# Kernel optimization log

Hardware: AMD Instinct MI355X
Metric: run time of the kernel (lower is better)

Reference implementation:

```python
import jax, jax.numpy as jnp
import numpy as np

N = 50000      # nodes
E = 800000     # edges (before self-loops)
F_IN = 64      # num_features
HID = 32       # hidden_channels
HEADS = 4
CLS = 3
NEG_SLOPE = 0.2  # PyG GATConv default


def setup_inputs() -> dict:
    key = jax.random.key(0)
    ks = jax.random.split(key, 12)
    s = 0.1
    return {
        "x": jax.random.normal(ks[0], (N, F_IN), jnp.float32),
        "W1": jax.random.normal(ks[1], (F_IN, HEADS * HID), jnp.float32) * s,
        "att_src1": jax.random.normal(ks[2], (HEADS, HID), jnp.float32) * s,
        "att_dst1": jax.random.normal(ks[3], (HEADS, HID), jnp.float32) * s,
        "b1": jnp.zeros((HEADS * HID,), jnp.float32),
        "W2": jax.random.normal(ks[4], (HEADS * HID, HID), jnp.float32) * s,
        "att_src2": jax.random.normal(ks[5], (1, HID), jnp.float32) * s,
        "att_dst2": jax.random.normal(ks[6], (1, HID), jnp.float32) * s,
        "b2": jnp.zeros((HID,), jnp.float32),
        "linW": jax.random.normal(ks[7], (HID, CLS), jnp.float32) * s,
        "linb": jnp.zeros((CLS,), jnp.float32),
        "edge_index": jax.random.randint(ks[8], (2, E), 0, N, dtype=jnp.int64),
    }


def _gat_conv(x, W, att_src, att_dst, bias, src, dst, heads):
    """PyG GATConv (eval mode, self-loops pre-added in src/dst)."""
    n = x.shape[0]
    h = (x @ W).reshape(n, heads, -1)                      # [N,H,C]
    a_src = jnp.sum(h * att_src, axis=-1)                  # [N,H]
    a_dst = jnp.sum(h * att_dst, axis=-1)                  # [N,H]
    e = jax.nn.leaky_relu(a_src[src] + a_dst[dst], NEG_SLOPE)  # [E,H]
    # segment softmax over destination node
    m = jax.ops.segment_max(e, dst, num_segments=n)
    p = jnp.exp(e - m[dst])
    denom = jax.ops.segment_sum(p, dst, num_segments=n)
    alpha = p / denom[dst]                                 # [E,H]
    msg = h[src] * alpha[:, :, None]                       # [E,H,C]
    out = jax.ops.segment_sum(msg, dst, num_segments=n)    # [N,H,C]
    return out.reshape(n, -1) + bias                       # concat heads


def reference(x, W1, att_src1, att_dst1, b1, W2, att_src2, att_dst2, b2, linW, linb, edge_index):
    n = x.shape[0]
    loop = jnp.arange(n, dtype=edge_index.dtype)
    src = jnp.concatenate([edge_index[0], loop])  # add self-loops (PyG default)
    dst = jnp.concatenate([edge_index[1], loop])
    h = _gat_conv(x, W1, att_src1, att_dst1, b1, src, dst, HEADS)
    h = jax.nn.elu(h)
    h = _gat_conv(h, W2, att_src2, att_dst2, b2, src, dst, 1)
    g = jnp.mean(h, axis=0, keepdims=True)        # batch is None path
    logits = g @ linW + linb                      # [1, CLS]
    return jax.nn.softmax(logits, axis=1)
```

## Files before the change

### kernel.cpp

```cpp
#include <hip/hip_runtime.h>
#include <hip/hip_fp16.h>
#include <math.h>

#define NEG_SLOPE 0.2f
#define CAP 64
#define SCB 2048

static __device__ __forceinline__ void atomAdd(float* a, float v) {
    unsafeAtomicAdd(a, v);
}

static __device__ __forceinline__ bool edges_are_i64(const int* __restrict__ ei) {
    return (ei[1] | ei[3] | ei[5] | ei[7]) == 0;
}
static __device__ __forceinline__ int ldsrc(const int* __restrict__ ei, int e, int E, bool i64) {
    return i64 ? ei[2 * e] : ei[e];
}
static __device__ __forceinline__ int lddst(const int* __restrict__ ei, int e, int E, bool i64) {
    return i64 ? ei[2 * (E + e)] : ei[E + e];
}

__global__ __launch_bounds__(256) void scatter_k(const int* __restrict__ ei,
                                                 int* __restrict__ deg,
                                                 int* __restrict__ col, int E, int N) {
    const int tid = threadIdx.x;
    const int grp = blockIdx.x & 7;
    const int bin = blockIdx.x >> 3;
    const int nb  = gridDim.x >> 3;
    const bool i64 = edges_are_i64(ei);
    const int ET = E + N;
    const int d0 = (int)((long long)grp * N / 8);
    const int d1 = (int)((long long)(grp + 1) * N / 8);
    for (int e = bin * 256 + tid; e < ET; e += nb * 256) {
        int s, d;
        if (e < E) { s = ldsrc(ei, e, E, i64); d = lddst(ei, e, E, i64); }
        else       { s = d = e - E; }
        if (d >= d0 && d < d1) {
            int pos = atomicAdd(&deg[d], 1);
            if (pos < CAP) col[d * CAP + pos] = s;
        }
    }
}

__global__ __launch_bounds__(256, 4) void gemm1_k(const float* __restrict__ x,
                                                  const float* __restrict__ W,
                                                  const float* __restrict__ aws,
                                                  const float* __restrict__ awd,
                                                  __half* __restrict__ h,
                                                  float* __restrict__ as_,
                                                  float* __restrict__ ad_, int N) {
    __shared__ float Ws[64 * 128];
    __shared__ float xs[32 * 64];
    const int tid = threadIdx.x;
    const int cg = tid & 31, rg = tid >> 5;
    const int r0 = blockIdx.x * 32;
#pragma unroll 1
    for (int i = tid; i < 8192; i += 256) Ws[i] = W[i];
    {
        const float* src = x + (size_t)r0 * 64;
        const int limit = (N - r0) * 64;
#pragma unroll 1
        for (int i = tid * 4; i < 2048; i += 1024) {
            float4 v = (i < limit) ? *(const float4*)(src + i) : make_float4(0, 0, 0, 0);
            *(float4*)(xs + i) = v;
        }
    }
    __syncthreads();

    float acc[4][4] = {};
#pragma unroll 2
    for (int k = 0; k < 64; k += 4) {
        float4 w0 = *(const float4*)(Ws + (k + 0) * 128 + cg * 4);
        float4 w1 = *(const float4*)(Ws + (k + 1) * 128 + cg * 4);
        float4 w2 = *(const float4*)(Ws + (k + 2) * 128 + cg * 4);
        float4 w3 = *(const float4*)(Ws + (k + 3) * 128 + cg * 4);
        float4 xv[4];
#pragma unroll
        for (int q = 0; q < 4; ++q) xv[q] = *(const float4*)(xs + (rg * 4 + q) * 64 + k);
#pragma unroll
        for (int q = 0; q < 4; ++q) {
            float4 xq = xv[q];
            acc[q][0] += xq.x * w0.x + xq.y * w1.x + xq.z * w2.x + xq.w * w3.x;
            acc[q][1] += xq.x * w0.y + xq.y * w1.y + xq.z * w2.y + xq.w * w3.y;
            acc[q][2] += xq.x * w0.z + xq.y * w1.z + xq.z * w2.z + xq.w * w3.z;
            acc[q][3] += xq.x * w0.w + xq.y * w1.w + xq.z * w2.w + xq.w * w3.w;
        }
    }

    const int jbase = cg * 4;
    const int head = cg >> 3;
    const float a0 = aws[jbase], a1 = aws[jbase + 1], a2 = aws[jbase + 2], a3 = aws[jbase + 3];
    const float d0 = awd[jbase], d1 = awd[jbase + 1], d2 = awd[jbase + 2], d3 = awd[jbase + 3];
    float ps[4], pd[4];
#pragma unroll
    for (int q = 0; q < 4; ++q) {
        ps[q] = acc[q][0] * a0 + acc[q][1] * a1 + acc[q][2] * a2 + acc[q][3] * a3;
        pd[q] = acc[q][0] * d0 + acc[q][1] * d1 + acc[q][2] * d2 + acc[q][3] * d3;
        int row = r0 + rg * 4 + q;
        if (row < N) {
            __half hv[4];
            hv[0] = __float2half(acc[q][0]); hv[1] = __float2half(acc[q][1]);
            hv[2] = __float2half(acc[q][2]); hv[3] = __float2half(acc[q][3]);
            *(uint2*)(h + (size_t)row * 128 + jbase) = *(uint2*)hv;
        }
    }
#pragma unroll
    for (int off = 4; off; off >>= 1) {
#pragma unroll
        for (int q = 0; q < 4; ++q) {
            ps[q] += __shfl_down(ps[q], off, 8);
            pd[q] += __shfl_down(pd[q], off, 8);
        }
    }
    if ((cg & 7) == 0) {
#pragma unroll
        for (int q = 0; q < 4; ++q) {
            int row = r0 + rg * 4 + q;
            if (row < N) { as_[row * 4 + head] = ps[q]; ad_[row * 4 + head] = pd[q]; }
        }
    }
}

__global__ __launch_bounds__(256, 4) void gemm2_k(const float* __restrict__ hact,
                                                  const float* __restrict__ W,
                                                  const float* __restrict__ aws,
                                                  const float* __restrict__ awd,
                                                  __half* __restrict__ h2,
                                                  float* __restrict__ as_,
                                                  float* __restrict__ ad_, int N) {
    __shared__ float Ws[128 * 32];
    __shared__ float xs[128 * 68];
    const int tid = threadIdx.x;
    const int cg = tid & 7, rg = tid >> 3;
    const int r0 = blockIdx.x * 128;
    for (int i = tid; i < 4096; i += 256) Ws[i] = W[i];

    float acc[4][4] = {};
#pragma unroll 1
    for (int p = 0; p < 2; ++p) {
        __syncthreads();
#pragma unroll 2
        for (int i = tid * 4; i < 8192; i += 1024) {
            int row = i >> 6, kk = i & 63;
            float4 v = (r0 + row < N)
                ? *(const float4*)(hact + (size_t)(r0 + row) * 128 + p * 64 + kk)
                : make_float4(0, 0, 0, 0);
            *(float4*)(xs + row * 68 + kk) = v;
        }
        __syncthreads();
#pragma unroll 2
        for (int k = 0; k < 64; k += 4) {
            float4 w0 = *(const float4*)(Ws + (p * 64 + k + 0) * 32 + cg * 4);
            float4 w1 = *(const float4*)(Ws + (p * 64 + k + 1) * 32 + cg * 4);
            float4 w2 = *(const float4*)(Ws + (p * 64 + k + 2) * 32 + cg * 4);
            float4 w3 = *(const float4*)(Ws + (p * 64 + k + 3) * 32 + cg * 4);
            float4 xv[4];
#pragma unroll
            for (int q = 0; q < 4; ++q) xv[q] = *(const float4*)(xs + (rg * 4 + q) * 68 + k);
#pragma unroll
            for (int q = 0; q < 4; ++q) {
                float4 xq = xv[q];
                acc[q][0] += xq.x * w0.x + xq.y * w1.x + xq.z * w2.x + xq.w * w3.x;
                acc[q][1] += xq.x * w0.y + xq.y * w1.y + xq.z * w2.y + xq.w * w3.y;
                acc[q][2] += xq.x * w0.z + xq.y * w1.z + xq.z * w2.z + xq.w * w3.z;
                acc[q][3] += xq.x * w0.w + xq.y * w1.w + xq.z * w2.w + xq.w * w3.w;
            }
        }
    }

    const int jbase = cg * 4;
    const float a0 = aws[jbase], a1 = aws[jbase + 1], a2 = aws[jbase + 2], a3 = aws[jbase + 3];
    const float d0 = awd[jbase], d1 = awd[jbase + 1], d2 = awd[jbase + 2], d3 = awd[jbase + 3];
    float ps[4], pd[4];
#pragma unroll
    for (int q = 0; q < 4; ++q) {
        ps[q] = acc[q][0] * a0 + acc[q][1] * a1 + acc[q][2] * a2 + acc[q][3] * a3;
        pd[q] = acc[q][0] * d0 + acc[q][1] * d1 + acc[q][2] * d2 + acc[q][3] * d3;
        int row = r0 + rg * 4 + q;
        if (row < N) {
            __half hv[4];
            hv[0] = __float2half(acc[q][0]); hv[1] = __float2half(acc[q][1]);
            hv[2] = __float2half(acc[q][2]); hv[3] = __float2half(acc[q][3]);
            *(uint2*)(h2 + (size_t)row * 32 + jbase) = *(uint2*)hv;
        }
    }
#pragma unroll
    for (int off = 4; off; off >>= 1) {
#pragma unroll
        for (int q = 0; q < 4; ++q) {
            ps[q] += __shfl_down(ps[q], off, 8);
            pd[q] += __shfl_down(pd[q], off, 8);
        }
    }
    if (cg == 0) {
#pragma unroll
        for (int q = 0; q < 4; ++q) {
            int row = r0 + rg * 4 + q;
            if (row < N) { as_[row] = ps[q]; ad_[row] = pd[q]; }
        }
    }
}

__global__ __launch_bounds__(256) void pull_agg1_k(const int* __restrict__ deg,
                                                   const int* __restrict__ col,
                                                   const float* __restrict__ asrc,
                                                   const float* __restrict__ adst,
                                                   const __half* __restrict__ h,
                                                   const float* __restrict__ b1,
                                                   float* __restrict__ hact, int N) {
    int wave = (blockIdx.x * 256 + threadIdx.x) >> 6;
    int lane = threadIdx.x & 63;
    if (wave >= N) return;
    const int d = wave;
    const int hd = lane >> 4;
    const float ad = adst[d * 4 + hd];
    const int* cl = col + d * CAP;
    int cnt = deg[d]; if (cnt > CAP) cnt = CAP;
    float acc0 = 0.0f, acc1 = 0.0f, den = 0.0f;
    int i = 0;
    for (; i + 8 <= cnt; i += 8) {
        int s[8]; float v[8]; __half2 g[8];
#pragma unroll
        for (int u = 0; u < 8; ++u) s[u] = cl[i + u];
#pragma unroll
        for (int u = 0; u < 8; ++u) v[u] = asrc[s[u] * 4 + hd] + ad;
#pragma unroll
        for (int u = 0; u < 8; ++u) g[u] = *(const __half2*)(h + (size_t)s[u] * 128 + lane * 2);
#pragma unroll
        for (int u = 0; u < 8; ++u) {
            float vv = v[u] > 0.0f ? v[u] : NEG_SLOPE * v[u];
            float p = __expf(vv);
            float2 gf = __half22float2(g[u]);
            den += p; acc0 += p * gf.x; acc1 += p * gf.y;
        }
    }
    for (; i < cnt; ++i) {
        int s = cl[i];
        float v = asrc[s * 4 + hd] + ad;
        v = v > 0.0f ? v : NEG_SLOPE * v;
        float p = __expf(v);
        float2 gf = __half22float2(*(const __half2*)(h + (size_t)s * 128 + lane * 2));
        den += p; acc0 += p * gf.x; acc1 += p * gf.y;
    }
    float inv = 1.0f / den;
    float o0 = acc0 * inv + b1[lane * 2];
    float o1 = acc1 * inv + b1[lane * 2 + 1];
    o0 = o0 > 0.0f ? o0 : expm1f(o0);
    o1 = o1 > 0.0f ? o1 : expm1f(o1);
    *(float2*)(hact + (size_t)d * 128 + lane * 2) = make_float2(o0, o1);
}

__global__ __launch_bounds__(256) void pull_agg2_k(const int* __restrict__ deg,
                                                   const int* __restrict__ col,
                                                   const float* __restrict__ asrc,
                                                   const float* __restrict__ adst,
                                                   const __half* __restrict__ h,
                                                   float* __restrict__ out, int N) {
    int grp = (blockIdx.x * 256 + threadIdx.x) >> 5;
    int lane = threadIdx.x & 31;
    if (grp >= N) return;
    const int d = grp;
    const float ad = adst[d];
    const int* cl = col + d * CAP;
    int cnt = deg[d]; if (cnt > CAP) cnt = CAP;
    float acc = 0.0f, den = 0.0f;
    int i = 0;
    for (; i + 8 <= cnt; i += 8) {
        int s[8]; float v[8]; __half g[8];
#pragma unroll
        for (int u = 0; u < 8; ++u) s[u] = cl[i + u];
#pragma unroll
        for (int u = 0; u < 8; ++u) v[u] = asrc[s[u]] + ad;
#pragma unroll
        for (int u = 0; u < 8; ++u) g[u] = h[(size_t)s[u] * 32 + lane];
#pragma unroll
        for (int u = 0; u < 8; ++u) {
            float vv = v[u] > 0.0f ? v[u] : NEG_SLOPE * v[u];
            float p = __expf(vv);
            den += p; acc += p * __half2float(g[u]);
        }
    }
    for (; i < cnt; ++i) {
        int s = cl[i];
        float v = asrc[s] + ad;
        v = v > 0.0f ? v : NEG_SLOPE * v;
        float p = __expf(v);
        den += p; acc += p * __half2float(h[(size_t)s * 32 + lane]);
    }
    out[(size_t)d * 32 + lane] = acc / den;
}

__global__ __launch_bounds__(256) void colmean_k(const float* __restrict__ out2,
                                                 float* __restrict__ gsum, int N) {
    __shared__ float lds[256];
    int tid = threadIdx.x;
    int c = tid % 32;
    int rg = tid / 32;
    float acc = 0.0f;
    for (int r = blockIdx.x * 8 + rg; r < N; r += gridDim.x * 8)
        acc += out2[(size_t)r * 32 + c];
    lds[tid] = acc;
    __syncthreads();
    if (tid < 32) {
        float s = 0.0f;
#pragma unroll
        for (int g = 0; g < 8; ++g) s += lds[g * 32 + tid];
        atomAdd(&gsum[tid], s);
    }
}

__global__ void final_k(const float* __restrict__ gsum, const float* __restrict__ b2w,
                        const float* __restrict__ linW, const float* __restrict__ linb,
                        float* __restrict__ out, int N) {
    if (threadIdx.x != 0 || blockIdx.x != 0) return;
    float g[32];
#pragma unroll
    for (int c = 0; c < 32; ++c) g[c] = gsum[c] / (float)N + b2w[c];
    float lo[3];
#pragma unroll
    for (int j = 0; j < 3; ++j) {
        float acc = linb[j];
#pragma unroll
        for (int c = 0; c < 32; ++c) acc += g[c] * linW[c * 3 + j];
        lo[j] = acc;
    }
    float mx = fmaxf(lo[0], fmaxf(lo[1], lo[2]));
    float ex[3], se = 0.0f;
#pragma unroll
    for (int j = 0; j < 3; ++j) { ex[j] = __expf(lo[j] - mx); se += ex[j]; }
#pragma unroll
    for (int j = 0; j < 3; ++j) out[j] = ex[j] / se;
}

extern "C" void kernel_launch(void* const* d_in, const int* in_sizes, int n_in,
                              void* d_out, int out_size, void* d_ws, size_t ws_size,
                              hipStream_t stream) {
    const float* x    = (const float*)d_in[0];
    const float* W1   = (const float*)d_in[1];
    const float* as1w = (const float*)d_in[2];
    const float* ad1w = (const float*)d_in[3];
    const float* b1   = (const float*)d_in[4];
    const float* W2   = (const float*)d_in[5];
    const float* as2w = (const float*)d_in[6];
    const float* ad2w = (const float*)d_in[7];
    const float* b2w  = (const float*)d_in[8];
    const float* linW = (const float*)d_in[9];
    const float* linb = (const float*)d_in[10];
    const int*   ei   = (const int*)d_in[11];

    const int N = in_sizes[0] / 64;
    const int E = in_sizes[11] / 2;

    float* ws = (float*)d_ws;
    __half* h1h  = (__half*)ws;
    float*  hact = ws + (size_t)N * 64;
    float* asrc1 = hact + (size_t)N * 128;
    float* adst1 = asrc1 + (size_t)N * 4;
    float* asrc2 = adst1 + (size_t)N * 4;
    float* adst2 = asrc2 + (size_t)N;
    float* gsum  = adst2 + (size_t)N;
    __half* h2h  = (__half*)ws;
    float*  out2 = ws + (size_t)N * 16;
    int* deg     = (int*)(gsum + 32);
    int* col     = deg + N;

    auto cdiv = [](int a, int b) { return (a + b - 1) / b; };

    hipMemsetAsync(deg, 0, (size_t)N * sizeof(int), stream);
    hipMemsetAsync(gsum, 0, 32 * sizeof(float), stream);

    scatter_k<<<SCB, 256, 0, stream>>>(ei, deg, col, E, N);

    gemm1_k<<<cdiv(N, 32), 256, 0, stream>>>(x, W1, as1w, ad1w, h1h, asrc1, adst1, N);
    pull_agg1_k<<<cdiv(N, 4), 256, 0, stream>>>(deg, col, asrc1, adst1, h1h, b1, hact, N);

    gemm2_k<<<cdiv(N, 128), 256, 0, stream>>>(hact, W2, as2w, ad2w, h2h, asrc2, adst2, N);
    pull_agg2_k<<<cdiv(N, 8), 256, 0, stream>>>(deg, col, asrc2, adst2, h2h, out2, N);

    colmean_k<<<256, 256, 0, stream>>>(out2, gsum, N);
    final_k<<<1, 64, 0, stream>>>(gsum, b2w, linW, linb, (float*)d_out, N);
}
```

Before: 247.0 us.

## Fuse layer-2 aggregation with mean and classifier, dedupe edge exp via shuffles

The layer-2 pull aggregation now folds its per-block column sums straight into padded global atomics. A last-block-done counter then runs the final linear and softmax, which removes the out2 buffer and the colmean and final kernels. In both aggregation kernels, each lane computes one edge's leaky-relu exp and broadcasts it with a shuffle, instead of every lane redundantly computing all eight. The two memsets are merged into one. In exchange, the change adds about 6250 block-level atomics and a threadfence/last-block pattern.

Result: slower. 393.7 us (+59.4%).

```diff
diff --git a/kernel.cpp b/kernel.cpp
--- a/kernel.cpp
+++ b/kernel.cpp
@@ -213,23 +213,25 @@
     if (wave >= N) return;
     const int d = wave;
     const int hd = lane >> 4;
+    const int sub = lane & 15;
     const float ad = adst[d * 4 + hd];
     const int* cl = col + d * CAP;
     int cnt = deg[d]; if (cnt > CAP) cnt = CAP;
     float acc0 = 0.0f, acc1 = 0.0f, den = 0.0f;
     int i = 0;
     for (; i + 8 <= cnt; i += 8) {
-        int s[8]; float v[8]; __half2 g[8];
+        int s[8];
 #pragma unroll
         for (int u = 0; u < 8; ++u) s[u] = cl[i + u];
-#pragma unroll
-        for (int u = 0; u < 8; ++u) v[u] = asrc[s[u] * 4 + hd] + ad;
+        float vmy = asrc[s[sub & 7] * 4 + hd] + ad;
+        vmy = vmy > 0.0f ? vmy : NEG_SLOPE * vmy;
+        float pmy = __expf(vmy);
+        __half2 g[8];
 #pragma unroll
         for (int u = 0; u < 8; ++u) g[u] = *(const __half2*)(h + (size_t)s[u] * 128 + lane * 2);
 #pragma unroll
         for (int u = 0; u < 8; ++u) {
-            float vv = v[u] > 0.0f ? v[u] : NEG_SLOPE * v[u];
-            float p = __expf(vv);
+            float p = __shfl(pmy, (lane & 48) | u, 64);
             float2 gf = __half22float2(g[u]);
             den += p; acc0 += p * gf.x; acc1 += p * gf.y;
         }
@@ -255,81 +257,86 @@
                                                    const float* __restrict__ asrc,
                                                    const float* __restrict__ adst,
                                                    const __half* __restrict__ h,
+                                                   float* __restrict__ gsumP,
+                                                   int* __restrict__ done,
+                                                   const float* __restrict__ b2w,
+                                                   const float* __restrict__ linW,
+                                                   const float* __restrict__ linb,
                                                    float* __restrict__ out, int N) {
-    int grp = (blockIdx.x * 256 + threadIdx.x) >> 5;
-    int lane = threadIdx.x & 31;
-    if (grp >= N) return;
-    const int d = grp;
-    const float ad = adst[d];
-    const int* cl = col + d * CAP;
-    int cnt = deg[d]; if (cnt > CAP) cnt = CAP;
-    float acc = 0.0f, den = 0.0f;
-    int i = 0;
-    for (; i + 8 <= cnt; i += 8) {
-        int s[8]; float v[8]; __half g[8];
-#pragma unroll
-        for (int u = 0; u < 8; ++u) s[u] = cl[i + u];
-#pragma unroll
-        for (int u = 0; u < 8; ++u) v[u] = asrc[s[u]] + ad;
-#pragma unroll
-        for (int u = 0; u < 8; ++u) g[u] = h[(size_t)s[u] * 32 + lane];
-#pragma unroll
-        for (int u = 0; u < 8; ++u) {
-            float vv = v[u] > 0.0f ? v[u] : NEG_SLOPE * v[u];
-            float p = __expf(vv);
-            den += p; acc += p * __half2float(g[u]);
-        }
-    }
-    for (; i < cnt; ++i) {
-        int s = cl[i];
-        float v = asrc[s] + ad;
-        v = v > 0.0f ? v : NEG_SLOPE * v;
-        float p = __expf(v);
-        den += p; acc += p * __half2float(h[(size_t)s * 32 + lane]);
-    }
-    out[(size_t)d * 32 + lane] = acc / den;
-}
-
-__global__ __launch_bounds__(256) void colmean_k(const float* __restrict__ out2,
-                                                 float* __restrict__ gsum, int N) {
-    __shared__ float lds[256];
-    int tid = threadIdx.x;
-    int c = tid % 32;
-    int rg = tid / 32;
-    float acc = 0.0f;
-    for (int r = blockIdx.x * 8 + rg; r < N; r += gridDim.x * 8)
-        acc += out2[(size_t)r * 32 + c];
-    lds[tid] = acc;
+    __shared__ float cs[256];
+    __shared__ int isLast;
+    const int tid = threadIdx.x;
+    const int lane = tid & 31;
+    const int grp = (blockIdx.x * 256 + tid) >> 5;
+    float val = 0.0f;
+    if (grp < N) {
+        const int d = grp;
+        const float ad = adst[d];
+        const int* cl = col + d * CAP;
+        int cnt = deg[d]; if (cnt > CAP) cnt = CAP;
+        float acc = 0.0f, den = 0.0f;
+        int i = 0;
+        const int wl = tid & 63;
+        for (; i + 8 <= cnt; i += 8) {
+            int s[8];
+#pragma unroll
+            for (int u = 0; u < 8; ++u) s[u] = cl[i + u];
+            float vmy = asrc[s[lane & 7]] + ad;
+            vmy = vmy > 0.0f ? vmy : NEG_SLOPE * vmy;
+            float pmy = __expf(vmy);
+            __half g[8];
+#pragma unroll
+            for (int u = 0; u < 8; ++u) g[u] = h[(size_t)s[u] * 32 + lane];
+#pragma unroll
+            for (int u = 0; u < 8; ++u) {
+                float p = __shfl(pmy, (wl & 32) | u, 64);
+                den += p; acc += p * __half2float(g[u]);
+            }
+        }
+        for (; i < cnt; ++i) {
+            int s = cl[i];
+            float v = asrc[s] + ad;
+            v = v > 0.0f ? v : NEG_SLOPE * v;
+            float p = __expf(v);
+            den += p; acc += p * __half2float(h[(size_t)s * 32 + lane]);
+        }
+        val = acc / den;
+    }
+    cs[tid] = val;
     __syncthreads();
     if (tid < 32) {
         float s = 0.0f;
 #pragma unroll
-        for (int g = 0; g < 8; ++g) s += lds[g * 32 + tid];
-        atomAdd(&gsum[tid], s);
-    }
-}
-
-__global__ void final_k(const float* __restrict__ gsum, const float* __restrict__ b2w,
-                        const float* __restrict__ linW, const float* __restrict__ linb,
-                        float* __restrict__ out, int N) {
-    if (threadIdx.x != 0 || blockIdx.x != 0) return;
-    float g[32];
-#pragma unroll
-    for (int c = 0; c < 32; ++c) g[c] = gsum[c] / (float)N + b2w[c];
-    float lo[3];
-#pragma unroll
-    for (int j = 0; j < 3; ++j) {
-        float acc = linb[j];
-#pragma unroll
-        for (int c = 0; c < 32; ++c) acc += g[c] * linW[c * 3 + j];
-        lo[j] = acc;
-    }
-    float mx = fmaxf(lo[0], fmaxf(lo[1], lo[2]));
-    float ex[3], se = 0.0f;
-#pragma unroll
-    for (int j = 0; j < 3; ++j) { ex[j] = __expf(lo[j] - mx); se += ex[j]; }
-#pragma unroll
-    for (int j = 0; j < 3; ++j) out[j] = ex[j] / se;
+        for (int g = 0; g < 8; ++g) s += cs[g * 32 + tid];
+        atomAdd(&gsumP[tid * 16], s);
+    }
+    __syncthreads();
+    if (tid == 0) {
+        __threadfence();
+        int old = atomicAdd(done, 1);
+        isLast = (old == (int)gridDim.x - 1);
+    }
+    __syncthreads();
+    if (isLast && tid == 0) {
+        __threadfence();
+        float g[32];
+#pragma unroll
+        for (int c = 0; c < 32; ++c) g[c] = gsumP[c * 16] / (float)N + b2w[c];
+        float lo[3];
+#pragma unroll
+        for (int j = 0; j < 3; ++j) {
+            float a = linb[j];
+#pragma unroll
+            for (int c = 0; c < 32; ++c) a += g[c] * linW[c * 3 + j];
+            lo[j] = a;
+        }
+        float mx = fmaxf(lo[0], fmaxf(lo[1], lo[2]));
+        float ex[3], se = 0.0f;
+#pragma unroll
+        for (int j = 0; j < 3; ++j) { ex[j] = __expf(lo[j] - mx); se += ex[j]; }
+#pragma unroll
+        for (int j = 0; j < 3; ++j) out[j] = ex[j] / se;
+    }
 }
 
 extern "C" void kernel_launch(void* const* d_in, const int* in_sizes, int n_in,
@@ -358,16 +365,15 @@
     float* adst1 = asrc1 + (size_t)N * 4;
     float* asrc2 = adst1 + (size_t)N * 4;
     float* adst2 = asrc2 + (size_t)N;
-    float* gsum  = adst2 + (size_t)N;
     __half* h2h  = (__half*)ws;
-    float*  out2 = ws + (size_t)N * 16;
-    int* deg     = (int*)(gsum + 32);
-    int* col     = deg + N;
+    float* gsumP = adst2 + (size_t)N;
+    int*   done  = (int*)(gsumP + 512);
+    int*   deg   = done + 8;
+    int*   col   = deg + N;
 
     auto cdiv = [](int a, int b) { return (a + b - 1) / b; };
 
-    hipMemsetAsync(deg, 0, (size_t)N * sizeof(int), stream);
-    hipMemsetAsync(gsum, 0, 32 * sizeof(float), stream);
+    hipMemsetAsync(gsumP, 0, (512 + 8 + (size_t)N) * 4, stream);
 
     scatter_k<<<SCB, 256, 0, stream>>>(ei, deg, col, E, N);
 
@@ -375,8 +381,7 @@
     pull_agg1_k<<<cdiv(N, 4), 256, 0, stream>>>(deg, col, asrc1, adst1, h1h, b1, hact, N);
 
     gemm2_k<<<cdiv(N, 128), 256, 0, stream>>>(hact, W2, as2w, ad2w, h2h, asrc2, adst2, N);
-    pull_agg2_k<<<cdiv(N, 8), 256, 0, stream>>>(deg, col, asrc2, adst2, h2h, out2, N);
-
-    colmean_k<<<256, 256, 0, stream>>>(out2, gsum, N);
-    final_k<<<1, 64, 0, stream>>>(gsum, b2w, linW, linb, (float*)d_out, N);
-}
+    pull_agg2_k<<<cdiv(N, 8), 256, 0, stream>>>(deg, col, asrc2, adst2, h2h,
+                                                gsumP, done, b2w, linW, linb,
+                                                (float*)d_out, N);
+}
```
